# Kernel optimization log

Measured on AMD Instinct MI355X. Metric: run time of the kernel, lower is better.

The kernel has to match this reference:

```python
import jax, jax.numpy as jnp
import numpy as np

B, C, H, W = 32, 256, 32, 32
HID, NPATH = 128, 4


def setup_inputs() -> dict:
    key = jax.random.key(0)
    ks = jax.random.split(key, 16)
    s = lambda *sh: 1.0 / np.sqrt(sh[-1])
    inp = {
        "lidar": jax.random.normal(ks[0], (B, C, H, W), jnp.float32),
        "hsi": jax.random.normal(ks[1], (B, C, H, W), jnp.float32),
        "x": jax.random.normal(ks[2], (B, C, H, W), jnp.float32),
        # shared Cross_Self_attention params
        "Wq": jax.random.normal(ks[3], (C, C), jnp.float32) * s(C, C),
        "bq": jnp.zeros((C,), jnp.float32),
        "Wk": jax.random.normal(ks[4], (C, C), jnp.float32) * s(C, C),
        "bk": jnp.zeros((C,), jnp.float32),
        "Wv": jax.random.normal(ks[5], (C, C), jnp.float32) * s(C, C),
        "bv": jnp.zeros((C,), jnp.float32),
        # 1x1 conv: [out=C, in=2C]
        "conv_w": jax.random.normal(ks[6], (C, 2 * C), jnp.float32) * s(C, 2 * C),
        "conv_b": jnp.zeros((C,), jnp.float32),
        # router MLP
        "r_w1": jax.random.normal(ks[7], (HID, 2 * C), jnp.float32) * s(HID, 2 * C),
        "r_b1": jnp.zeros((HID,), jnp.float32),
        "r_w2": jax.random.normal(ks[8], (NPATH, HID), jnp.float32) * s(NPATH, HID),
        "r_b2": jnp.zeros((NPATH,), jnp.float32),
    }
    return inp


def _cross_self_attn(xq, yv, Wq, bq, Wk, bk, Wv, bv):
    # xq, yv: [b, s, c]
    q = xq @ Wq.T + bq
    k = xq @ Wk.T + bk
    v = yv @ Wv.T + bv
    probs = jax.nn.softmax(jnp.einsum("bsc,btc->bst", q, k), axis=-1)  # [b,s,s]
    return jnp.einsum("bst,btc->bsc", probs, q * v)  # bilinear value Q*V


def reference(lidar, hsi, x, Wq, bq, Wk, bk, Wv, bv, conv_w, conv_b, r_w1, r_b1, r_w2, r_b2):
    b, c, h, w = lidar.shape
    # Router: concat channels, spatial mean pool, MLP, sigmoid
    g = jnp.concatenate([lidar, hsi], axis=1).mean(axis=(2, 3))  # [b, 2c]
    path_prob = jax.nn.sigmoid(jax.nn.relu(g @ r_w1.T + r_b1) @ r_w2.T + r_b2)

    l = lidar.reshape(b, c, h * w).transpose(0, 2, 1)  # b (h w) c
    hh = hsi.reshape(b, c, h * w).transpose(0, 2, 1)

    h_emb = _cross_self_attn(l, hh, Wq, bq, Wk, bk, Wv, bv)  # [b, hw, c]
    l_emb = _cross_self_attn(hh, l, Wq, bq, Wk, bk, Wv, bv)

    h_emb = h_emb.transpose(0, 2, 1).reshape(b, c, h, w)
    l_emb = l_emb.transpose(0, 2, 1).reshape(b, c, h, w)

    cat = jnp.concatenate([l_emb, h_emb], axis=1)  # [b, 2c, h, w]
    emb = jnp.einsum("bihw,oi->bohw", cat, conv_w) + conv_b[None, :, None, None] + x
    return emb, path_prob
```

## Files before the change

kernel.cpp:

```cpp
#include <hip/hip_runtime.h>
#include <stdint.h>

typedef unsigned short u16;
typedef unsigned int u32;
typedef _Float16 f16;
typedef _Float16 f16x8 __attribute__((ext_vector_type(8)));
typedef _Float16 f16x4 __attribute__((ext_vector_type(4)));
typedef float f32x4 __attribute__((ext_vector_type(4)));
typedef float f32x16 __attribute__((ext_vector_type(16)));

#define B_ 32
#define C_ 256
#define S_ 1024

__global__ __launch_bounds__(256) void k_mlp(
    const float* __restrict__ g,
    const float* __restrict__ w1, const float* __restrict__ b1,
    const float* __restrict__ w2, const float* __restrict__ b2,
    float* __restrict__ out)
{
    int b = blockIdx.x, tid = threadIdx.x;
    __shared__ float sg[512];
    __shared__ float sh[128];
    sg[tid]     = g[b*512 + tid]       * (1.0f/1024.0f);
    sg[tid+256] = g[b*512 + 256 + tid] * (1.0f/1024.0f);
    __syncthreads();
    if (tid < 128){
        float a = b1[tid];
        const float* w = w1 + (size_t)tid*512;
        #pragma unroll 4
        for (int k = 0; k < 512; k += 4){
            float4 wv = *(const float4*)(w + k);
            a += sg[k]*wv.x + sg[k+1]*wv.y + sg[k+2]*wv.z + sg[k+3]*wv.w;
        }
        sh[tid] = fmaxf(a, 0.f);
    }
    __syncthreads();
    if (tid < 4){
        float a = b2[tid];
        const float* w = w2 + (size_t)tid*128;
        for (int k = 0; k < 128; ++k) a += sh[k]*w[k];
        out[(size_t)8388608 + b*4 + tid] = 1.f/(1.f+expf(-a));
    }
}

__global__ __launch_bounds__(256) void k_cvtw(
    const float* __restrict__ Wq, const float* __restrict__ Wk,
    const float* __restrict__ Wv, const float* __restrict__ cw,
    f16* __restrict__ Wqf, f16* __restrict__ Wkf,
    f16* __restrict__ Wvf, f16* __restrict__ cwf)
{
    int i = (blockIdx.x*256 + threadIdx.x) * 4;
    const float* src; f16* dst; int off;
    if (i < 65536){ src = Wq; dst = Wqf; off = i; }
    else if (i < 131072){ src = Wk; dst = Wkf; off = i - 65536; }
    else if (i < 196608){ src = Wv; dst = Wvf; off = i - 131072; }
    else { src = cw; dst = cwf; off = i - 196608; }
    float4 v = *(const float4*)(src + off);
    f16x4 r = { (f16)v.x, (f16)v.y, (f16)v.z, (f16)v.w };
    *(f16x4*)(dst + off) = r;
}

__global__ __launch_bounds__(256) void k_cvt(
    const float* __restrict__ lidar, const float* __restrict__ hsi,
    f16* __restrict__ lidT, f16* __restrict__ hsiT,
    float* __restrict__ g)
{
    int z = blockIdx.z, which = z >> 5, b = z & 31;
    const float* src = (which ? hsi : lidar) + (size_t)b*C_*S_;
    f16* dst = (which ? hsiT : lidT) + (size_t)b*S_*C_;
    int tid = threadIdx.x;
    int c4 = blockIdx.y*64 + (tid&15)*4;
    int s4 = blockIdx.x*64 + (tid>>4)*4;
    float4 m[4];
    #pragma unroll
    for (int r = 0; r < 4; ++r) m[r] = *(const float4*)(src + (size_t)(c4+r)*S_ + s4);
    f16x4 t0 = { (f16)m[0].x, (f16)m[1].x, (f16)m[2].x, (f16)m[3].x };
    f16x4 t1 = { (f16)m[0].y, (f16)m[1].y, (f16)m[2].y, (f16)m[3].y };
    f16x4 t2 = { (f16)m[0].z, (f16)m[1].z, (f16)m[2].z, (f16)m[3].z };
    f16x4 t3 = { (f16)m[0].w, (f16)m[1].w, (f16)m[2].w, (f16)m[3].w };
    *(f16x4*)(dst + (size_t)(s4+0)*C_ + c4) = t0;
    *(f16x4*)(dst + (size_t)(s4+1)*C_ + c4) = t1;
    *(f16x4*)(dst + (size_t)(s4+2)*C_ + c4) = t2;
    *(f16x4*)(dst + (size_t)(s4+3)*C_ + c4) = t3;
    float ps[4];
    #pragma unroll
    for (int r = 0; r < 4; ++r){
        ps[r] = m[r].x + m[r].y + m[r].z + m[r].w;
        ps[r] += __shfl_xor(ps[r], 16, 64);
        ps[r] += __shfl_xor(ps[r], 32, 64);
    }
    __shared__ float sred[4][64];
    int wv = tid>>6, lane = tid&63;
    if ((lane>>4) == 0){
        #pragma unroll
        for (int r = 0; r < 4; ++r) sred[wv][(lane&15)*4 + r] = ps[r];
    }
    __syncthreads();
    if (tid < 64){
        float v = sred[0][tid] + sred[1][tid] + sred[2][tid] + sred[3][tid];
        atomicAdd(&g[b*512 + which*256 + blockIdx.y*64 + tid], v);
    }
}

__global__ __launch_bounds__(256) void k_qkv(
    const f16* __restrict__ lidT, const f16* __restrict__ hsiT,
    const f16* __restrict__ Wqf, const f16* __restrict__ Wkf, const f16* __restrict__ Wvf,
    const float* __restrict__ bq, const float* __restrict__ bk, const float* __restrict__ bv,
    f16* __restrict__ Qf_l, f16* __restrict__ Kf_l,
    f16* __restrict__ Qf_h, f16* __restrict__ Kf_h,
    f16* __restrict__ Qt_l, f16* __restrict__ Qt_h,
    f16* __restrict__ Vt_l, f16* __restrict__ Vt_h)
{
    int z = blockIdx.z, combo = z >> 5, b = z & 31, ww = combo % 3;
    const f16* In = ((combo < 3) ? lidT : hsiT) + (size_t)b*S_*C_;
    const f16* Wf = (ww==0) ? Wqf : (ww==1) ? Wkf : Wvf;
    const float* bias = (ww==0) ? bq : (ww==1) ? bk : bv;
    int s0 = blockIdx.x*128, o0 = blockIdx.y*64;
    int tid = threadIdx.x, w = tid>>6, lane = tid&63, quad = lane>>4, l15 = lane&15;

    __shared__ __align__(16) f16 sA[128*72];
    __shared__ __align__(16) f16 sB[64*72];

    f32x4 D[2][4];
    #pragma unroll
    for (int h = 0; h < 2; ++h)
        #pragma unroll
        for (int i = 0; i < 4; ++i) D[h][i] = (f32x4){0.f,0.f,0.f,0.f};

    int rowA = tid>>1, cA = (tid&1)*32;
    int rowB = tid>>2, cB = (tid&3)*16;
    for (int c0 = 0; c0 < 256; c0 += 64){
        __syncthreads();
        #pragma unroll
        for (int j = 0; j < 4; ++j)
            *(f16x8*)&sA[rowA*72 + cA + 8*j] = *(const f16x8*)(In + (size_t)(s0+rowA)*C_ + c0 + cA + 8*j);
        #pragma unroll
        for (int j = 0; j < 2; ++j)
            *(f16x8*)&sB[rowB*72 + cB + 8*j] = *(const f16x8*)(Wf + (size_t)(o0+rowB)*C_ + c0 + cB + 8*j);
        __syncthreads();
        #pragma unroll
        for (int sub = 0; sub < 2; ++sub){
            f16x8 a0 = *(const f16x8*)&sA[(w*16+l15)*72 + sub*32 + quad*8];
            f16x8 a1 = *(const f16x8*)&sA[((w+4)*16+l15)*72 + sub*32 + quad*8];
            #pragma unroll
            for (int bt = 0; bt < 4; ++bt){
                f16x8 bb = *(const f16x8*)&sB[(bt*16+l15)*72 + sub*32 + quad*8];
                D[0][bt] = __builtin_amdgcn_mfma_f32_16x16x32_f16(a0, bb, D[0][bt], 0,0,0);
                D[1][bt] = __builtin_amdgcn_mfma_f32_16x16x32_f16(a1, bb, D[1][bt], 0,0,0);
            }
        }
    }
    float bi[4];
    #pragma unroll
    for (int bt = 0; bt < 4; ++bt) bi[bt] = bias[o0 + bt*16 + l15];

    if (ww != 2){
        f16* F = (ww==0) ? ((combo==0) ? Qf_l : Qf_h) : ((combo==1) ? Kf_l : Kf_h);
        F += (size_t)b*S_*C_;
        #pragma unroll
        for (int h = 0; h < 2; ++h)
            #pragma unroll
            for (int bt = 0; bt < 4; ++bt)
                #pragma unroll
                for (int r = 0; r < 4; ++r)
                    F[(size_t)(s0 + h*64 + w*16 + quad*4 + r)*C_ + o0 + bt*16 + l15] = (f16)(D[h][bt][r] + bi[bt]);
    }
    if (ww != 1){
        __syncthreads();
        #pragma unroll
        for (int h = 0; h < 2; ++h)
            #pragma unroll
            for (int bt = 0; bt < 4; ++bt)
                #pragma unroll
                for (int r = 0; r < 4; ++r)
                    sA[(bt*16+l15)*136 + h*64 + w*16 + quad*4 + r] = (f16)(D[h][bt][r] + bi[bt]);
        __syncthreads();
        f16* T = (combo==0) ? Qt_l : (combo==3) ? Qt_h : (combo==2) ? Vt_l : Vt_h;
        T += (size_t)b*C_*S_;
        int o_r = tid>>2, sc = (tid&3)*32;
        #pragma unroll
        for (int j = 0; j < 4; ++j)
            *(f16x8*)(T + (size_t)(o0+o_r)*S_ + s0 + sc + 8*j) = *(const f16x8*)&sA[o_r*136 + sc + 8*j];
    }
}

__global__ __launch_bounds__(256) void k_qv(
    const f16* __restrict__ Qt_l, const f16* __restrict__ Qt_h,
    const f16* __restrict__ Vt_l, const f16* __restrict__ Vt_h,
    f16* __restrict__ QVT1, f16* __restrict__ QVT2)
{
    size_t idx = (size_t)(blockIdx.x*256 + threadIdx.x) * 8;
    f16x8 a = *(const f16x8*)(Qt_l+idx);
    f16x8 b = *(const f16x8*)(Vt_h+idx);
    *(f16x8*)(QVT1+idx) = a*b;
    f16x8 c = *(const f16x8*)(Qt_h+idx);
    f16x8 d = *(const f16x8*)(Vt_l+idx);
    *(f16x8*)(QVT2+idx) = c*d;
}

__global__ __launch_bounds__(256, 2) void k_attn(
    const f16* __restrict__ Qf_l, const f16* __restrict__ Kf_l,
    const f16* __restrict__ Qf_h, const f16* __restrict__ Kf_h,
    const f16* __restrict__ QVT1, const f16* __restrict__ QVT2,
    f16* __restrict__ cat)
{
    int inst = blockIdx.y;
    int b = inst >> 1, which = inst & 1;
    const f16* Qf  = (which ? Qf_h : Qf_l) + (size_t)b*S_*C_;
    const f16* Kf  = (which ? Kf_h : Kf_l) + (size_t)b*S_*C_;
    const f16* QVT = (which ? QVT2 : QVT1) + (size_t)b*C_*S_;
    f16* outp = cat + (size_t)b*S_*512 + (which ? 0 : 256);
    int s0 = blockIdx.x*64;
    int tid = threadIdx.x, w = tid>>6, lane = tid&63;
    int l31 = lane&31, b5 = lane>>5;
    int sh2 = w&1, hf = w>>1;

    __shared__ __align__(16) f16 sV[256*72];
    __shared__ __align__(16) f16 sP[64*72];
    __shared__ float sRm[2][64], sRl[2][64];
    __shared__ float sSt[64][2];

    f16x8 qB[16];
    {
        const f16* qbase = Qf + (size_t)(s0 + 32*sh2 + l31)*C_ + b5*8;
        #pragma unroll
        for (int k = 0; k < 16; ++k) qB[k] = *(const f16x8*)(qbase + k*16);
    }
    if (tid < 64){ sSt[tid][0] = -1e30f; sSt[tid][1] = 0.f; }

    f32x16 pacc[4];
    #pragma unroll
    for (int i = 0; i < 4; ++i) pacc[i] = (f32x16)(0.f);

    const f16* kbase = Kf + (size_t)(32*hf + l31)*C_ + b5*8;
    int smy = 32*sh2 + l31;

    for (int tt = 0; tt < 16; ++tt){
        int t0 = tt*64;
        __syncthreads();
        #pragma unroll
        for (int p = 0; p < 8; ++p){
            int idx = p*256 + tid; int row = idx>>3, t8 = (idx&7)*8;
            *(f16x8*)&sV[row*72 + t8] = *(const f16x8*)(QVT + (size_t)row*S_ + t0 + t8);
        }
        f16x8 kA[16];
        {
            const f16* kb = kbase + (size_t)t0*C_;
            #pragma unroll
            for (int k = 0; k < 16; ++k) kA[k] = *(const f16x8*)(kb + k*16);
        }
        __syncthreads();

        f32x16 St = (f32x16)(0.f);
        #pragma unroll
        for (int k = 0; k < 16; ++k)
            St = __builtin_amdgcn_mfma_f32_32x32x16_f16(kA[k], qB[k], St, 0,0,0);

        float tmax = St[0];
        #pragma unroll
        for (int i = 1; i < 16; ++i) tmax = fmaxf(tmax, St[i]);
        tmax = fmaxf(tmax, __shfl_xor(tmax, 32, 64));
        if (lane < 32) sRm[hf][32*sh2 + lane] = tmax;
        __syncthreads();

        float mo = sSt[smy][0];
        float mn = fmaxf(mo, fmaxf(sRm[0][smy], sRm[1][smy]));
        float p16[16];
        float ls = 0.f;
        #pragma unroll
        for (int i = 0; i < 16; ++i){ p16[i] = __expf(St[i] - mn); ls += p16[i]; }
        #pragma unroll
        for (int g = 0; g < 4; ++g){
            f16x4 pk = { (f16)p16[4*g], (f16)p16[4*g+1], (f16)p16[4*g+2], (f16)p16[4*g+3] };
            *(f16x4*)&sP[smy*72 + 32*hf + 8*g + 4*b5] = pk;
        }
        ls += __shfl_xor(ls, 32, 64);
        if (lane < 32) sRl[hf][32*sh2 + lane] = ls;
        __syncthreads();

        float alpha = __expf(mo - mn);
        if (hf == 0 && lane < 32){
            float ln = sSt[smy][1]*alpha + sRl[0][smy] + sRl[1][smy];
            sSt[smy][0] = mn; sSt[smy][1] = ln;
        }
        #pragma unroll
        for (int ct = 0; ct < 4; ++ct)
            #pragma unroll
            for (int i = 0; i < 16; ++i) pacc[ct][i] *= alpha;

        #pragma unroll
        for (int kp = 0; kp < 4; ++kp){
            f16x8 pB = *(const f16x8*)&sP[smy*72 + kp*16 + b5*8];
            #pragma unroll
            for (int ct = 0; ct < 4; ++ct){
                f16x8 vA = *(const f16x8*)&sV[(128*hf + 32*ct + l31)*72 + kp*16 + b5*8];
                pacc[ct] = __builtin_amdgcn_mfma_f32_32x32x16_f16(vA, pB, pacc[ct], 0,0,0);
            }
        }
    }

    __syncthreads();
    float rl = 1.f / sSt[smy][1];
    f16* sE = sV;
    #pragma unroll
    for (int ct = 0; ct < 4; ++ct)
        #pragma unroll
        for (int i = 0; i < 16; ++i){
            int cl = 128*hf + 32*ct + (i&3) + 8*(i>>2) + 4*b5;
            sE[(32*sh2 + l31)*264 + cl] = (f16)(pacc[ct][i] * rl);
        }
    __syncthreads();
    {
        int s = tid>>2;
        #pragma unroll
        for (int i = 0; i < 8; ++i){
            int c8 = ((tid&3) + 4*i)*8;
            *(f16x8*)(outp + (size_t)(s0+s)*512 + c8) = *(const f16x8*)&sE[s*264 + c8];
        }
    }
}

__global__ __launch_bounds__(256) void k_conv(
    const f16* __restrict__ cat, const f16* __restrict__ cwf,
    const float* __restrict__ cb, const float* __restrict__ x,
    float* __restrict__ out)
{
    int b = blockIdx.z;
    int s0 = blockIdx.x*64, o0 = blockIdx.y*128;
    int tid = threadIdx.x, w = tid>>6, lane = tid&63, quad = lane>>4, l15 = lane&15;

    __shared__ __align__(16) f16 sA[128*72];
    __shared__ __align__(16) f16 sB[64*72];

    f32x4 D[2][4];
    #pragma unroll
    for (int h = 0; h < 2; ++h)
        #pragma unroll
        for (int i = 0; i < 4; ++i) D[h][i] = (f32x4){0.f,0.f,0.f,0.f};

    const f16* catb = cat + (size_t)b*S_*512;
    int rowA = tid>>1, iA = (tid&1)*32;
    int rowB = tid>>2, iB = (tid&3)*16;
    for (int i0 = 0; i0 < 512; i0 += 64){
        __syncthreads();
        #pragma unroll
        for (int j = 0; j < 4; ++j)
            *(f16x8*)&sA[rowA*72 + iA + 8*j] = *(const f16x8*)(cwf + (size_t)(o0+rowA)*512 + i0 + iA + 8*j);
        #pragma unroll
        for (int j = 0; j < 2; ++j)
            *(f16x8*)&sB[rowB*72 + iB + 8*j] = *(const f16x8*)(catb + (size_t)(s0+rowB)*512 + i0 + iB + 8*j);
        __syncthreads();
        #pragma unroll
        for (int sub = 0; sub < 2; ++sub){
            f16x8 a0 = *(const f16x8*)&sA[(w*16+l15)*72 + sub*32 + quad*8];
            f16x8 a1 = *(const f16x8*)&sA[((w+4)*16+l15)*72 + sub*32 + quad*8];
            #pragma unroll
            for (int bt = 0; bt < 4; ++bt){
                f16x8 bb = *(const f16x8*)&sB[(bt*16+l15)*72 + sub*32 + quad*8];
                D[0][bt] = __builtin_amdgcn_mfma_f32_16x16x32_f16(a0, bb, D[0][bt], 0,0,0);
                D[1][bt] = __builtin_amdgcn_mfma_f32_16x16x32_f16(a1, bb, D[1][bt], 0,0,0);
            }
        }
    }
    #pragma unroll
    for (int h = 0; h < 2; ++h)
        #pragma unroll
        for (int r = 0; r < 4; ++r){
            int o_loc = h*64 + w*16 + quad*4 + r;
            float cbv = cb[o0 + o_loc];
            size_t base = (size_t)b*C_*S_ + (size_t)(o0+o_loc)*S_ + s0;
            #pragma unroll
            for (int bt = 0; bt < 4; ++bt){
                size_t a = base + bt*16 + l15;
                out[a] = D[h][bt][r] + cbv + x[a];
            }
        }
}

extern "C" void kernel_launch(void* const* d_in, const int* in_sizes, int n_in,
                              void* d_out, int out_size, void* d_ws, size_t ws_size,
                              hipStream_t stream)
{
    const float* lidar = (const float*)d_in[0];
    const float* hsi   = (const float*)d_in[1];
    const float* x     = (const float*)d_in[2];
    const float* Wq = (const float*)d_in[3];  const float* bq = (const float*)d_in[4];
    const float* Wk = (const float*)d_in[5];  const float* bk = (const float*)d_in[6];
    const float* Wv = (const float*)d_in[7];  const float* bv = (const float*)d_in[8];
    const float* cw = (const float*)d_in[9];  const float* cb = (const float*)d_in[10];
    const float* rw1 = (const float*)d_in[11]; const float* rb1 = (const float*)d_in[12];
    const float* rw2 = (const float*)d_in[13]; const float* rb2 = (const float*)d_in[14];
    float* outF = (float*)d_out;
    char* ws = (char*)d_ws;
    const size_t M = 1ull<<20;

    f16* lidT = (f16*)(ws +   0*M);
    f16* hsiT = (f16*)(ws +  16*M);
    f16* Qf_l = (f16*)(ws +  32*M);
    f16* Kf_l = (f16*)(ws +  48*M);
    f16* Qf_h = (f16*)(ws +  64*M);
    f16* Kf_h = (f16*)(ws +  80*M);
    f16* Qt_l = (f16*)(ws +  96*M);
    f16* Qt_h = (f16*)(ws + 112*M);
    f16* cat  = (f16*)(ws + 128*M);
    float* g  = (float*)(ws + 160*M);
    f16* Wqf  = (f16*)(ws + 161*M);
    f16* Wkf  = (f16*)(ws + 161*M + 131072);
    f16* Wvf  = (f16*)(ws + 161*M + 262144);
    f16* cwf  = (f16*)(ws + 161*M + 393216);
    f16* QVT1 = lidT;
    f16* QVT2 = hsiT;
    f16* Vt_l = (f16*)d_out;
    f16* Vt_h = (f16*)d_out + 8388608;

    hipMemsetAsync(g, 0, 4096*sizeof(float), stream);
    k_cvtw<<<320, 256, 0, stream>>>(Wq, Wk, Wv, cw, Wqf, Wkf, Wvf, cwf);
    k_cvt<<<dim3(16,4,64), 256, 0, stream>>>(lidar, hsi, lidT, hsiT, g);
    k_mlp<<<32, 256, 0, stream>>>(g, rw1, rb1, rw2, rb2, outF);
    k_qkv<<<dim3(8,4,192), 256, 0, stream>>>(lidT, hsiT, Wqf, Wkf, Wvf, bq, bk, bv,
                                             Qf_l, Kf_l, Qf_h, Kf_h, Qt_l, Qt_h, Vt_l, Vt_h);
    k_qv<<<4096, 256, 0, stream>>>(Qt_l, Qt_h, Vt_l, Vt_h, QVT1, QVT2);
    k_attn<<<dim3(16,64), 256, 0, stream>>>(Qf_l, Kf_l, Qf_h, Kf_h, QVT1, QVT2, cat);
    k_conv<<<dim3(16,2,32), 256, 0, stream>>>(cat, cwf, cb, x, outF);
}
```

Measured before the change: 438.4 us.

## Restructure attention kernel: 128-row query tiles, per-wave softmax, swizzled LDS K/V

Each attention block now handles 128 query rows, one 32-row slice per wave, instead of 64 rows split across wave pairs. Online softmax state stays in registers, which removes the cross-wave shared-memory reductions and two of the barriers per key tile. K tiles are staged in XOR-swizzled LDS shared by all waves, and the rescale of the accumulators is skipped when the running max does not change. Block indices are remapped so that neighbouring blocks work on different batch instances. In exchange each thread keeps 8 accumulator tiles and LDS use grows to 80KB, which may lower occupancy and increase register pressure.

```diff
diff --git a/kernel.cpp b/kernel.cpp
--- a/kernel.cpp
+++ b/kernel.cpp
@@ -205,118 +205,128 @@
     const f16* __restrict__ QVT1, const f16* __restrict__ QVT2,
     f16* __restrict__ cat)
 {
-    int inst = blockIdx.y;
+    int bid = blockIdx.x;
+    int inst = ((bid & 7) << 3) | ((bid >> 3) & 7);
+    int sb = bid >> 6;
     int b = inst >> 1, which = inst & 1;
     const f16* Qf  = (which ? Qf_h : Qf_l) + (size_t)b*S_*C_;
     const f16* Kf  = (which ? Kf_h : Kf_l) + (size_t)b*S_*C_;
     const f16* QVT = (which ? QVT2 : QVT1) + (size_t)b*C_*S_;
     f16* outp = cat + (size_t)b*S_*512 + (which ? 0 : 256);
-    int s0 = blockIdx.x*64;
+    int s0 = sb*128;
     int tid = threadIdx.x, w = tid>>6, lane = tid&63;
     int l31 = lane&31, b5 = lane>>5;
-    int sh2 = w&1, hf = w>>1;
-
-    __shared__ __align__(16) f16 sV[256*72];
-    __shared__ __align__(16) f16 sP[64*72];
-    __shared__ float sRm[2][64], sRl[2][64];
-    __shared__ float sSt[64][2];
+
+    __shared__ __align__(16) char smem[81920];
+    f16* sK  = (f16*)smem;
+    f16* sV  = (f16*)(smem + 32768);
+    f16* sPw = (f16*)(smem + 65536) + w*2048;
 
     f16x8 qB[16];
     {
-        const f16* qbase = Qf + (size_t)(s0 + 32*sh2 + l31)*C_ + b5*8;
-        #pragma unroll
-        for (int k = 0; k < 16; ++k) qB[k] = *(const f16x8*)(qbase + k*16);
-    }
-    if (tid < 64){ sSt[tid][0] = -1e30f; sSt[tid][1] = 0.f; }
-
-    f32x16 pacc[4];
-    #pragma unroll
-    for (int i = 0; i < 4; ++i) pacc[i] = (f32x16)(0.f);
-
-    const f16* kbase = Kf + (size_t)(32*hf + l31)*C_ + b5*8;
-    int smy = 32*sh2 + l31;
+        const f16* qrow = Qf + (size_t)(s0 + 32*w + l31)*C_ + b5*8;
+        #pragma unroll
+        for (int ks = 0; ks < 16; ++ks) qB[ks] = *(const f16x8*)(qrow + ks*16);
+    }
+    float mrun = -1e30f, lrun = 0.f;
+    f32x16 pacc[8];
+    #pragma unroll
+    for (int i = 0; i < 8; ++i) pacc[i] = (f32x16)(0.f);
 
     for (int tt = 0; tt < 16; ++tt){
         int t0 = tt*64;
         __syncthreads();
         #pragma unroll
         for (int p = 0; p < 8; ++p){
-            int idx = p*256 + tid; int row = idx>>3, t8 = (idx&7)*8;
-            *(f16x8*)&sV[row*72 + t8] = *(const f16x8*)(QVT + (size_t)row*S_ + t0 + t8);
-        }
-        f16x8 kA[16];
-        {
-            const f16* kb = kbase + (size_t)t0*C_;
-            #pragma unroll
-            for (int k = 0; k < 16; ++k) kA[k] = *(const f16x8*)(kb + k*16);
-        }
-        __syncthreads();
-
-        f32x16 St = (f32x16)(0.f);
-        #pragma unroll
-        for (int k = 0; k < 16; ++k)
-            St = __builtin_amdgcn_mfma_f32_32x32x16_f16(kA[k], qB[k], St, 0,0,0);
-
-        float tmax = St[0];
-        #pragma unroll
-        for (int i = 1; i < 16; ++i) tmax = fmaxf(tmax, St[i]);
+            int idx = p*256 + tid;
+            int t = idx >> 5, c8 = idx & 31;
+            *(f16x8*)&sK[t*256 + ((c8 ^ (t&31))<<3)] =
+                *(const f16x8*)(Kf + (size_t)(t0+t)*C_ + c8*8);
+        }
+        #pragma unroll
+        for (int p = 0; p < 8; ++p){
+            int idx = p*256 + tid;
+            int c = idx >> 3, t8 = idx & 7;
+            *(f16x8*)&sV[c*64 + ((t8 ^ (c&7))<<3)] =
+                *(const f16x8*)(QVT + (size_t)c*S_ + t0 + t8*8);
+        }
+        __syncthreads();
+
+        f32x16 St0 = (f32x16)(0.f), St1 = (f32x16)(0.f);
+        #pragma unroll
+        for (int ks = 0; ks < 16; ++ks){
+            int c8 = ks*2 + b5;
+            f16x8 kA0 = *(const f16x8*)&sK[l31*256      + ((c8 ^ l31)<<3)];
+            f16x8 kA1 = *(const f16x8*)&sK[(32+l31)*256 + ((c8 ^ l31)<<3)];
+            St0 = __builtin_amdgcn_mfma_f32_32x32x16_f16(kA0, qB[ks], St0, 0,0,0);
+            St1 = __builtin_amdgcn_mfma_f32_32x32x16_f16(kA1, qB[ks], St1, 0,0,0);
+        }
+
+        float tmax = St0[0];
+        #pragma unroll
+        for (int i = 1; i < 16; ++i) tmax = fmaxf(tmax, St0[i]);
+        #pragma unroll
+        for (int i = 0; i < 16; ++i) tmax = fmaxf(tmax, St1[i]);
         tmax = fmaxf(tmax, __shfl_xor(tmax, 32, 64));
-        if (lane < 32) sRm[hf][32*sh2 + lane] = tmax;
-        __syncthreads();
-
-        float mo = sSt[smy][0];
-        float mn = fmaxf(mo, fmaxf(sRm[0][smy], sRm[1][smy]));
-        float p16[16];
+        float mo = mrun;
+        float mn = fmaxf(mo, tmax);
         float ls = 0.f;
-        #pragma unroll
-        for (int i = 0; i < 16; ++i){ p16[i] = __expf(St[i] - mn); ls += p16[i]; }
-        #pragma unroll
-        for (int g = 0; g < 4; ++g){
-            f16x4 pk = { (f16)p16[4*g], (f16)p16[4*g+1], (f16)p16[4*g+2], (f16)p16[4*g+3] };
-            *(f16x4*)&sP[smy*72 + 32*hf + 8*g + 4*b5] = pk;
+        f16x4 pk[2][4];
+        #pragma unroll
+        for (int i = 0; i < 16; ++i){
+            float p0 = __expf(St0[i] - mn); ls += p0; pk[0][i>>2][i&3] = (f16)p0;
+            float p1 = __expf(St1[i] - mn); ls += p1; pk[1][i>>2][i&3] = (f16)p1;
         }
         ls += __shfl_xor(ls, 32, 64);
-        if (lane < 32) sRl[hf][32*sh2 + lane] = ls;
-        __syncthreads();
-
-        float alpha = __expf(mo - mn);
-        if (hf == 0 && lane < 32){
-            float ln = sSt[smy][1]*alpha + sRl[0][smy] + sRl[1][smy];
-            sSt[smy][0] = mn; sSt[smy][1] = ln;
-        }
-        #pragma unroll
-        for (int ct = 0; ct < 4; ++ct)
-            #pragma unroll
-            for (int i = 0; i < 16; ++i) pacc[ct][i] *= alpha;
+        float al = __expf(mo - mn);
+        mrun = mn;
+        lrun = lrun*al + ls;
+        #pragma unroll
+        for (int tg = 0; tg < 2; ++tg)
+            #pragma unroll
+            for (int rq = 0; rq < 4; ++rq){
+                int t8 = tg*4 + rq;
+                *(f16x4*)&sPw[l31*64 + ((t8 ^ (l31&7))<<3) + 4*b5] = pk[tg][rq];
+            }
+        if (!__all(mo == mn)){
+            #pragma unroll
+            for (int cg = 0; cg < 8; ++cg)
+                #pragma unroll
+                for (int i = 0; i < 16; ++i) pacc[cg][i] *= al;
+        }
 
         #pragma unroll
         for (int kp = 0; kp < 4; ++kp){
-            f16x8 pB = *(const f16x8*)&sP[smy*72 + kp*16 + b5*8];
-            #pragma unroll
-            for (int ct = 0; ct < 4; ++ct){
-                f16x8 vA = *(const f16x8*)&sV[(128*hf + 32*ct + l31)*72 + kp*16 + b5*8];
-                pacc[ct] = __builtin_amdgcn_mfma_f32_32x32x16_f16(vA, pB, pacc[ct], 0,0,0);
+            int t8 = kp*2 + b5;
+            f16x8 pB = *(const f16x8*)&sPw[l31*64 + ((t8 ^ (l31&7))<<3)];
+            #pragma unroll
+            for (int cg = 0; cg < 8; ++cg){
+                int c = cg*32 + l31;
+                f16x8 vA = *(const f16x8*)&sV[c*64 + ((t8 ^ (c&7))<<3)];
+                pacc[cg] = __builtin_amdgcn_mfma_f32_32x32x16_f16(vA, pB, pacc[cg], 0,0,0);
             }
         }
     }
 
     __syncthreads();
-    float rl = 1.f / sSt[smy][1];
-    f16* sE = sV;
-    #pragma unroll
-    for (int ct = 0; ct < 4; ++ct)
-        #pragma unroll
-        for (int i = 0; i < 16; ++i){
-            int cl = 128*hf + 32*ct + (i&3) + 8*(i>>2) + 4*b5;
-            sE[(32*sh2 + l31)*264 + cl] = (f16)(pacc[ct][i] * rl);
+    float rl = 1.f / lrun;
+    f16* sE = (f16*)smem + w*8448;
+    #pragma unroll
+    for (int cg = 0; cg < 8; ++cg)
+        #pragma unroll
+        for (int rq = 0; rq < 4; ++rq){
+            int c = cg*32 + rq*8 + 4*b5;
+            f16x4 v = { (f16)(pacc[cg][rq*4+0]*rl), (f16)(pacc[cg][rq*4+1]*rl),
+                        (f16)(pacc[cg][rq*4+2]*rl), (f16)(pacc[cg][rq*4+3]*rl) };
+            *(f16x4*)&sE[l31*264 + c] = v;
         }
     __syncthreads();
     {
-        int s = tid>>2;
-        #pragma unroll
-        for (int i = 0; i < 8; ++i){
-            int c8 = ((tid&3) + 4*i)*8;
-            *(f16x8*)(outp + (size_t)(s0+s)*512 + c8) = *(const f16x8*)&sE[s*264 + c8];
+        int sl = lane>>1;
+        #pragma unroll
+        for (int i = 0; i < 16; ++i){
+            int c = (lane&1)*128 + i*8;
+            *(f16x8*)(outp + (size_t)(s0 + 32*w + sl)*512 + c) = *(const f16x8*)&sE[sl*264 + c];
         }
     }
 }
@@ -421,6 +431,6 @@
     k_qkv<<<dim3(8,4,192), 256, 0, stream>>>(lidT, hsiT, Wqf, Wkf, Wvf, bq, bk, bv,
                                              Qf_l, Kf_l, Qf_h, Kf_h, Qt_l, Qt_h, Vt_l, Vt_h);
     k_qv<<<4096, 256, 0, stream>>>(Qt_l, Qt_h, Vt_l, Vt_h, QVT1, QVT2);
-    k_attn<<<dim3(16,64), 256, 0, stream>>>(Qf_l, Kf_l, Qf_h, Kf_h, QVT1, QVT2, cat);
+    k_attn<<<512, 256, 0, stream>>>(Qf_l, Kf_l, Qf_h, Kf_h, QVT1, QVT2, cat);
     k_conv<<<dim3(16,2,32), 256, 0, stream>>>(cat, cwf, cb, x, outF);
 }
```

Result: slower. 535.5 us (+22.1%).
